# Optimization experiments

Measured on AMD Instinct MI355X. Metric: run time of the kernel, lower is better.

The kernel has to match this reference:

```python
import jax, jax.numpy as jnp
import numpy as np

B, F_C, F_F = 2, 32768, 131072
C_IN, C_OUT, W_DIM, COLOR = 128, 64, 512, 3
K2 = 9
PAD0, PAD1 = 192, 384
ACT_GAIN = float(np.sqrt(2.0))  # lrelu def_gain


def _gather(x, nbr, is_pad, pad):
    # x: [N, C]; nbr: [M, k] indices into [N + pad]; is_pad: [M, k] bool
    padded = jnp.concatenate([x, jnp.zeros((pad, x.shape[1]), x.dtype)], 0)
    g = padded[nbr]  # [M, k, C]
    return jnp.where(is_pad[..., None], jnp.zeros((), x.dtype), g)


def _affine(w, aw, ab):
    # StyleGAN FullyConnectedLayer: runtime weight gain 1/sqrt(fan_in), bias_init=1
    return w @ (aw.T * (1.0 / np.sqrt(aw.shape[1]))) + ab


def _modconv(xg, weight, styles, demodulate=True):
    # xg: [N, k, I]; weight: [O, I, 1, k]; styles: [B, I]
    n, k, ci = xg.shape
    w = weight[:, :, 0, :][None, :, :, :] * styles[:, None, :, None]  # [B,O,I,k]
    if demodulate:
        w = w * jax.lax.rsqrt(jnp.sum(w * w, axis=(2, 3), keepdims=True) + 1e-8)
    xb = xg.reshape(styles.shape[0], -1, k, ci)  # [B,F,k,I]
    return jnp.einsum('bfki,boik->bfo', xb, w).reshape(n, -1)


def _smooth_upsample(x, nbr, is_pad, pad, pool_map):
    # upsample coarse->fine via parent map, then masked neighborhood mean
    xf = x[pool_map]  # [N_fine, C]
    g = _gather(xf, nbr, is_pad, pad)  # [N_fine, k, C]
    cnt = jnp.maximum(jnp.sum(~is_pad, axis=1), 1).astype(x.dtype)
    return jnp.sum(g, axis=1) / cnt[:, None]


def _act(x, gain):
    # clamp_gain(lrelu(x), act_gain*gain, 256*gain)
    y = jnp.where(x >= 0, x, 0.2 * x)
    return jnp.clip(y * (ACT_GAIN * gain), -256.0 * gain, 256.0 * gain)


def setup_inputs():
    key = jax.random.key(0)
    ks = jax.random.split(key, 16)
    x = jax.random.normal(ks[0], (B * F_C, C_IN), jnp.float32)
    img = jax.random.normal(ks[1], (B * F_C, COLOR), jnp.float32)
    ws = jax.random.normal(ks[2], (B, 3, W_DIM), jnp.float32)
    fn0 = jax.random.randint(ks[3], (B * F_C, K2), 0, B * F_C + PAD0, jnp.int32)
    fn1 = jax.random.randint(ks[4], (B * F_F, K2), 0, B * F_F + PAD1, jnp.int32)
    fip0 = jax.random.bernoulli(ks[5], 0.05, (B * F_C, K2))
    fip1 = jax.random.bernoulli(ks[6], 0.05, (B * F_F, K2))
    pool_map0 = jax.random.randint(ks[7], (B * F_F,), 0, B * F_C, jnp.int32)
    a0_w = jax.random.normal(ks[8], (C_IN, W_DIM), jnp.float32)
    a0_b = jnp.ones((C_IN,), jnp.float32)
    W0 = jax.random.normal(ks[9], (C_OUT, C_IN, 1, K2), jnp.float32)
    b0 = jnp.zeros((C_OUT,), jnp.float32)
    ns0 = jnp.zeros((1,), jnp.float32)
    nc0 = jax.random.normal(ks[10], (F_F,), jnp.float32)
    a1_w = jax.random.normal(ks[11], (C_OUT, W_DIM), jnp.float32)
    a1_b = jnp.ones((C_OUT,), jnp.float32)
    W1 = jax.random.normal(ks[12], (C_OUT, C_OUT, 1, K2), jnp.float32)
    b1 = jnp.zeros((C_OUT,), jnp.float32)
    ns1 = jnp.zeros((1,), jnp.float32)
    nc1 = jax.random.normal(ks[13], (F_F,), jnp.float32)
    at_w = jax.random.normal(ks[14], (C_OUT, W_DIM), jnp.float32)
    at_b = jnp.ones((C_OUT,), jnp.float32)
    Wt = jax.random.normal(ks[15], (COLOR, C_OUT, 1, 1), jnp.float32)
    bt = jnp.zeros((COLOR,), jnp.float32)
    return {"x": x, "img": img, "ws": ws, "a0_w": a0_w, "a0_b": a0_b, "W0": W0,
            "b0": b0, "ns0": ns0, "nc0": nc0, "a1_w": a1_w, "a1_b": a1_b,
            "W1": W1, "b1": b1, "ns1": ns1, "nc1": nc1, "at_w": at_w,
            "at_b": at_b, "Wt": Wt, "bt": bt, "fn0": fn0, "fip0": fip0,
            "fn1": fn1, "fip1": fip1, "pool_map0": pool_map0,
            "pad0": PAD0, "pad1": PAD1}


def reference(x, img, ws, a0_w, a0_b, W0, b0, ns0, nc0, a1_w, a1_b, W1, b1, ns1,
              nc1, at_w, at_b, Wt, bt, fn0, fip0, fn1, fip1, pool_map0, pad0, pad1):
    b = ws.shape[0]
    w0, w1, w2 = ws[:, 0], ws[:, 1], ws[:, 2]
    # conv0: coarse gather -> mod conv -> smooth upsample to fine -> noise/bias/act
    s0 = _affine(w0, a0_w, a0_b)
    noise0 = jnp.tile(nc0[None, :], (b, 1)).reshape(-1, 1) * ns0  # noise_mode='const'
    h = _modconv(_gather(x, fn0, fip0, pad0), W0, s0)
    h = _smooth_upsample(h, fn1, fip1, pad1, pool_map0)
    h = _act(h + noise0 + b0[None, :], 1.0)
    # conv1: fine level, no resampler
    s1 = _affine(w1, a1_w, a1_b)
    noise1 = jnp.tile(nc1[None, :], (b, 1)).reshape(-1, 1) * ns1
    h = _modconv(_gather(h, fn1, fip1, pad1), W1, s1)
    h = _act(h + noise1 + b1[None, :], 1.0)
    # torgb: kernel_size=1 -> self index only, no demodulation
    st = _affine(w2, at_w, at_b) * (1.0 / np.sqrt(C_OUT))
    y = _modconv(_gather(h, fn1[:, :1], fip1[:, :1], pad1), Wt, st, demodulate=False)
    y = jnp.clip(y + bt[None, :], -256.0, 256.0)
    img = _smooth_upsample(img, fn1, fip1, pad1, pool_map0) + y
    return (h, img)
```

## Files before the change

kernel.cpp:

```cpp
#include <hip/hip_runtime.h>
#include <hip/hip_bf16.h>

constexpr int F_C   = 32768;
constexpr int F_F   = 131072;
constexpr int N0    = 65536;
constexpr int N1    = 262144;
constexpr int C_IN  = 128;
constexpr int W_DIM = 512;
constexpr int K2c   = 9;
constexpr float RS512     = 0.04419417382415922f;
constexpr float ACT_GAINc = 1.4142135623730951f;

constexpr size_t FO_S0  = 0;
constexpr size_t FO_S1  = 256;
constexpr size_t FO_ST  = 384;
constexpr size_t OFF_WM0T = 2048;
constexpr size_t OFF_WM1T = OFF_WM0T + 294912;
constexpr size_t OFF_H0   = 458752;
constexpr size_t OFF_HA   = OFF_H0 + (size_t)8388608;
constexpr size_t OFF_YPRE = OFF_H0;

typedef short s16x8 __attribute__((ext_vector_type(8)));
typedef float f32x4 __attribute__((ext_vector_type(4)));

__device__ __forceinline__ float b2f(unsigned short u) {
    union { unsigned int i; float f; } v; v.i = ((unsigned int)u) << 16; return v.f;
}
__device__ __forceinline__ unsigned short f2b(float f) {
    __hip_bfloat16 h = __float2bfloat16(f);
    return *reinterpret_cast<unsigned short*>(&h);
}
__device__ __forceinline__ float waveRedSum(float v) {
    for (int m = 32; m; m >>= 1) v += __shfl_xor(v, m, 64);
    return v;
}
__device__ __forceinline__ float actf(float v) {
    float y = (v >= 0.f) ? v : 0.2f * v;
    y *= ACT_GAINc;
    return fminf(fmaxf(y, -256.f), 256.f);
}

__global__ __launch_bounds__(64)
void k_styles(const float* __restrict__ wsF,
              const float* __restrict__ a0w, const float* __restrict__ a0b,
              const float* __restrict__ a1w, const float* __restrict__ a1b,
              const float* __restrict__ atw, const float* __restrict__ atb,
              float* __restrict__ fr)
{
    int bid = blockIdx.x, lane = threadIdx.x;
    int bb, ii, ll, row; const float *aw, *ab; float* dst; float post = 1.f;
    if (bid < 256)      { bb = bid >> 7;             ii = bid & 127; ll = 0; aw = a0w; ab = a0b; dst = fr + FO_S0; row = 128; }
    else if (bid < 384) { int t = bid - 256; bb = t >> 6; ii = t & 63; ll = 1; aw = a1w; ab = a1b; dst = fr + FO_S1; row = 64; }
    else                { int t = bid - 384; bb = t >> 6; ii = t & 63; ll = 2; aw = atw; ab = atb; dst = fr + FO_ST; row = 64; post = 0.125f; }
    const float* wsv = wsF + (size_t)(bb * 3 + ll) * W_DIM;
    const float* awr = aw + (size_t)ii * W_DIM;
    float s = 0.f;
    for (int j = lane; j < W_DIM; j += 64) s += wsv[j] * awr[j];
    s = waveRedSum(s);
    if (lane == 0) dst[bb * row + ii] = (s * RS512 + ab[ii]) * post;
}

__global__ __launch_bounds__(256)
void k_wmod(const float* __restrict__ W0,
            const float* __restrict__ W1,
            const float* __restrict__ fr,
            unsigned short* __restrict__ wm0T,
            unsigned short* __restrict__ wm1T)
{
    int bo = blockIdx.x, tid = threadIdx.x;
    int b, o, CI, NE; const float* W; const float* S; unsigned short* dst;
    if (bo < 128) { b = bo >> 6; o = bo & 63; CI = 128; NE = 1152; W = W0; S = fr + FO_S0; dst = wm0T; }
    else { int t = bo - 128; b = t >> 6; o = t & 63; CI = 64; NE = 576; W = W1; S = fr + FO_S1; dst = wm1T; }
    const float* Wo = W + (size_t)o * NE;
    const float* Sb = S + (size_t)b * CI;
    float ss = 0.f;
    for (int idx = tid; idx < NE; idx += 256) {
        int i = idx / K2c;
        float p = Wo[idx] * Sb[i];
        ss += p * p;
    }
    __shared__ float red[4];
    float s = waveRedSum(ss);
    if ((tid & 63) == 0) red[tid >> 6] = s;
    __syncthreads();
    float d = rsqrtf(red[0] + red[1] + red[2] + red[3] + 1e-8f);
    for (int idx = tid; idx < NE; idx += 256) {
        int i = idx / K2c, kk = idx - i * K2c;
        dst[((size_t)(b * K2c + kk) * 64 + o) * CI + i] = f2b(Wo[idx] * Sb[i] * d);
    }
}

__global__ __launch_bounds__(256)
void k_layer0(const float* __restrict__ xF,
              const int*  __restrict__ fn0,
              const int*  __restrict__ fip0,
              const unsigned short* __restrict__ wm0T,
              unsigned short* __restrict__ h0B)
{
    __shared__ unsigned short A_lds[64 * 136];
    __shared__ unsigned short W_lds[64 * 136];
    __shared__ int snbr[64];
    const int tid  = threadIdx.x;
    const int g0   = blockIdx.x * 64;
    const int b    = g0 / F_C;
    const int wave = tid >> 6, lane = tid & 63;
    const int lg   = lane >> 4, lr = lane & 15;
    f32x4 acc[4] = {};
    for (int kk = 0; kk < K2c; ++kk) {
        __syncthreads();
        if (tid < 64) {
            int g   = g0 + tid;
            int nbr = fn0[(size_t)g * K2c + kk];
            int pd  = fip0[(size_t)g * K2c + kk];
            snbr[tid] = (!pd && nbr < N0) ? nbr : -1;
        }
        __syncthreads();
        {
            int node = tid >> 2, seg = tid & 3;
            int nbr  = snbr[node];
            unsigned short tmp[32];
            if (nbr >= 0) {
                const float4* src = (const float4*)(xF + (size_t)nbr * C_IN + seg * 32);
                #pragma unroll
                for (int q = 0; q < 8; ++q) {
                    float4 f = src[q];
                    tmp[q*4+0] = f2b(f.x); tmp[q*4+1] = f2b(f.y);
                    tmp[q*4+2] = f2b(f.z); tmp[q*4+3] = f2b(f.w);
                }
            } else {
                #pragma unroll
                for (int q = 0; q < 32; ++q) tmp[q] = 0;
            }
            uint4* dstA = (uint4*)(A_lds + node * 136 + seg * 32);
            #pragma unroll
            for (int q = 0; q < 4; ++q) dstA[q] = ((const uint4*)tmp)[q];
            const uint4* wsrc = (const uint4*)(wm0T + ((size_t)(b * K2c + kk) * 64 + node) * C_IN + seg * 32);
            uint4* dstW = (uint4*)(W_lds + node * 136 + seg * 32);
            #pragma unroll
            for (int q = 0; q < 4; ++q) dstW[q] = wsrc[q];
        }
        __syncthreads();
        #pragma unroll
        for (int ks = 0; ks < 4; ++ks) {
            int kb = ks * 32 + lg * 8;
            s16x8 af = *(const s16x8*)(A_lds + (wave * 16 + lr) * 136 + kb);
            #pragma unroll
            for (int nt = 0; nt < 4; ++nt) {
                s16x8 bf = *(const s16x8*)(W_lds + (nt * 16 + lr) * 136 + kb);
                acc[nt] = __builtin_amdgcn_mfma_f32_16x16x32_bf16(af, bf, acc[nt], 0, 0, 0);
            }
        }
    }
    #pragma unroll
    for (int nt = 0; nt < 4; ++nt) {
        int o = nt * 16 + lr;
        #pragma unroll
        for (int r = 0; r < 4; ++r) {
            int node = g0 + wave * 16 + lg * 4 + r;
            h0B[(size_t)node * 64 + o] = f2b(acc[nt][r]);
        }
    }
}

__global__ __launch_bounds__(256)
void k_ha(const unsigned short* __restrict__ h0B,
          const int*  __restrict__ fn1,
          const int*  __restrict__ fip1,
          const int*  __restrict__ pool,
          const float* __restrict__ nc0,
          const float* __restrict__ ns0,
          const float* __restrict__ b0,
          unsigned short* __restrict__ haB)
{
    __shared__ int   pmArr[288];
    __shared__ int   vArr[288];
    __shared__ float invCnt[32];
    const int tid = threadIdx.x;
    const int n0  = blockIdx.x * 32;
    for (int idx = tid; idx < 288; idx += 256) {
        int fn = fn1[(size_t)n0 * K2c + idx];
        int ip = fip1[(size_t)n0 * K2c + idx];
        int v  = !ip;
        int pm = -1;
        if (v && fn < N1) pm = pool[fn];
        pmArr[idx] = pm;
        vArr[idx]  = v;
    }
    __syncthreads();
    if (tid < 32) {
        int c = 0;
        #pragma unroll
        for (int k = 0; k < K2c; ++k) c += vArr[tid * K2c + k];
        invCnt[tid] = 1.f / (float)(c > 0 ? c : 1);
    }
    __syncthreads();
    const int wave = tid >> 6, lane = tid & 63;
    const float nsc  = ns0[0];
    const float bias = b0[lane];
    for (int jj = 0; jj < 8; ++jj) {
        int node = wave * 8 + jj;
        int g    = n0 + node;
        float acc = 0.f;
        #pragma unroll
        for (int k = 0; k < K2c; ++k) {
            int pm = pmArr[node * K2c + k];
            int pc = pm >= 0 ? pm : 0;
            float val = b2f(h0B[(size_t)pc * 64 + lane]);
            acc += (pm >= 0) ? val : 0.f;
        }
        float hu = acc * invCnt[node];
        float v  = hu + nc0[g & (F_F - 1)] * nsc + bias;
        haB[(size_t)g * 64 + lane] = f2b(actf(v));
    }
}

__global__ __launch_bounds__(256)
void k_layer1(const unsigned short* __restrict__ haB,
              const int*  __restrict__ fn1,
              const int*  __restrict__ fip1,
              const unsigned short* __restrict__ wm1T,
              const float* __restrict__ nc1,
              const float* __restrict__ ns1,
              const float* __restrict__ b1,
              const float* __restrict__ stS,
              const float* __restrict__ WtF,
              float* __restrict__ hOut,
              float* __restrict__ yPre2)
{
    __shared__ unsigned short W_lds[2][64 * 72];
    __shared__ int snbr[576];
    const int tid  = threadIdx.x;
    const int g0   = blockIdx.x * 64;
    const int b    = g0 / F_F;
    const int wave = tid >> 6, lane = tid & 63;
    const int lg   = lane >> 4, lr = lane & 15;

    const unsigned short* wtap = wm1T + (size_t)b * K2c * 64 * 64;

    for (int idx = tid; idx < 576; idx += 256) {
        int fn = fn1[(size_t)g0 * K2c + idx];
        int ip = fip1[(size_t)g0 * K2c + idx];
        snbr[idx] = (!ip && fn < N1) ? fn : -1;
    }
    {
        const uint4* src = (const uint4*)wtap;
        int s0 = tid * 2, s1 = s0 + 1;
        uint4 v0 = src[s0], v1 = src[s1];
        *(uint4*)(&W_lds[0][(s0 >> 3) * 72 + (s0 & 7) * 8]) = v0;
        *(uint4*)(&W_lds[0][(s1 >> 3) * 72 + (s1 & 7) * 8]) = v1;
    }
    __syncthreads();

    const int row = wave * 16 + lr;
    int nbrk[9];
    #pragma unroll
    for (int k = 0; k < 9; ++k) nbrk[k] = snbr[row * 9 + k];

    f32x4 acc[4] = {};
    #pragma unroll
    for (int kk = 0; kk < 9; ++kk) {
        const int cur = kk & 1;
        int nbr = nbrk[kk];
        int pc  = nbr >= 0 ? nbr : 0;
        const uint4* ap = (const uint4*)(haB + (size_t)pc * 64) + lg;
        uint4 a0 = ap[0];
        uint4 a1 = ap[4];
        if (nbr < 0) { a0 = uint4{0,0,0,0}; a1 = uint4{0,0,0,0}; }
        if (kk < 8) {
            const uint4* src = (const uint4*)(wtap + (size_t)(kk + 1) * 4096);
            int s0 = tid * 2, s1 = s0 + 1;
            uint4 v0 = src[s0], v1 = src[s1];
            *(uint4*)(&W_lds[cur ^ 1][(s0 >> 3) * 72 + (s0 & 7) * 8]) = v0;
            *(uint4*)(&W_lds[cur ^ 1][(s1 >> 3) * 72 + (s1 & 7) * 8]) = v1;
        }
        s16x8 af0 = *reinterpret_cast<const s16x8*>(&a0);
        s16x8 af1 = *reinterpret_cast<const s16x8*>(&a1);
        #pragma unroll
        for (int nt = 0; nt < 4; ++nt) {
            s16x8 bf0 = *(const s16x8*)(&W_lds[cur][(nt * 16 + lr) * 72 + lg * 8]);
            acc[nt] = __builtin_amdgcn_mfma_f32_16x16x32_bf16(af0, bf0, acc[nt], 0, 0, 0);
        }
        #pragma unroll
        for (int nt = 0; nt < 4; ++nt) {
            s16x8 bf1 = *(const s16x8*)(&W_lds[cur][(nt * 16 + lr) * 72 + 32 + lg * 8]);
            acc[nt] = __builtin_amdgcn_mfma_f32_16x16x32_bf16(af1, bf1, acc[nt], 0, 0, 0);
        }
        __syncthreads();
    }

    float nsc = ns1[0];
    float p00[4] = {}, p01[4] = {}, p02[4] = {};
    float p10[4] = {}, p11[4] = {}, p12[4] = {};
    #pragma unroll
    for (int nt = 0; nt < 4; ++nt) {
        int o = nt * 16 + lr;
        float bias = b1[o];
        float st0  = stS[o], st1 = stS[64 + o];
        float wt0 = WtF[o], wt1 = WtF[64 + o], wt2 = WtF[128 + o];
        float w00 = wt0 * st0, w01 = wt1 * st0, w02 = wt2 * st0;
        float w10 = wt0 * st1, w11 = wt1 * st1, w12 = wt2 * st1;
        #pragma unroll
        for (int r = 0; r < 4; ++r) {
            int node = g0 + wave * 16 + lg * 4 + r;
            float v  = actf(acc[nt][r] + nc1[node & (F_F - 1)] * nsc + bias);
            hOut[(size_t)node * 64 + o] = v;
            p00[r] += v * w00; p01[r] += v * w01; p02[r] += v * w02;
            p10[r] += v * w10; p11[r] += v * w11; p12[r] += v * w12;
        }
    }
    #pragma unroll
    for (int m = 1; m < 16; m <<= 1) {
        #pragma unroll
        for (int r = 0; r < 4; ++r) {
            p00[r] += __shfl_xor(p00[r], m, 64);
            p01[r] += __shfl_xor(p01[r], m, 64);
            p02[r] += __shfl_xor(p02[r], m, 64);
            p10[r] += __shfl_xor(p10[r], m, 64);
            p11[r] += __shfl_xor(p11[r], m, 64);
            p12[r] += __shfl_xor(p12[r], m, 64);
        }
    }
    if (lr == 0) {
        #pragma unroll
        for (int r = 0; r < 4; ++r) {
            int node = g0 + wave * 16 + lg * 4 + r;
            yPre2[(size_t)node * 6 + 0] = p00[r];
            yPre2[(size_t)node * 6 + 1] = p01[r];
            yPre2[(size_t)node * 6 + 2] = p02[r];
            yPre2[(size_t)node * 6 + 3] = p10[r];
            yPre2[(size_t)node * 6 + 4] = p11[r];
            yPre2[(size_t)node * 6 + 5] = p12[r];
        }
    }
}

__global__ __launch_bounds__(256)
void k_rgb(const float* __restrict__ yPre2,
           const float* __restrict__ imgF,
           const int*  __restrict__ fn1,
           const int*  __restrict__ fip1,
           const int*  __restrict__ pool,
           const float* __restrict__ btF,
           float* __restrict__ outImg)
{
    const int n = blockIdx.x * 256 + threadIdx.x;
    const int bOut = n / F_F;
    int fn[K2c], ip[K2c];
    #pragma unroll
    for (int k = 0; k < K2c; ++k) {
        fn[k] = fn1[(size_t)n * K2c + k];
        ip[k] = fip1[(size_t)n * K2c + k];
    }
    int pm[K2c], cnt = 0;
    #pragma unroll
    for (int k = 0; k < K2c; ++k) {
        int v  = !ip[k];
        cnt   += v;
        pm[k]  = (v && fn[k] < N1) ? pool[fn[k]] : -1;
    }
    float sr = 0.f, sg = 0.f, sb = 0.f;
    #pragma unroll
    for (int k = 0; k < K2c; ++k) {
        int   pc = pm[k] >= 0 ? pm[k] : 0;
        float m  = pm[k] >= 0 ? 1.f : 0.f;
        sr += m * imgF[(size_t)pc * 3 + 0];
        sg += m * imgF[(size_t)pc * 3 + 1];
        sb += m * imgF[(size_t)pc * 3 + 2];
    }
    int nb0 = (!ip[0] && fn[0] < N1) ? fn[0] : -1;
    float y0 = 0.f, y1 = 0.f, y2 = 0.f;
    if (nb0 >= 0) {
        const float* yp = yPre2 + (size_t)nb0 * 6 + bOut * 3;
        y0 = yp[0]; y1 = yp[1]; y2 = yp[2];
    }
    float ic = 1.f / (float)(cnt > 0 ? cnt : 1);
    y0 = fminf(fmaxf(y0 + btF[0], -256.f), 256.f);
    y1 = fminf(fmaxf(y1 + btF[1], -256.f), 256.f);
    y2 = fminf(fmaxf(y2 + btF[2], -256.f), 256.f);
    outImg[(size_t)n * 3 + 0] = sr * ic + y0;
    outImg[(size_t)n * 3 + 1] = sg * ic + y1;
    outImg[(size_t)n * 3 + 2] = sb * ic + y2;
}

extern "C" void kernel_launch(void* const* d_in, const int* in_sizes, int n_in,
                              void* d_out, int out_size, void* d_ws, size_t ws_size,
                              hipStream_t stream)
{
    const float* xF   = (const float*)d_in[0];
    const float* imgF = (const float*)d_in[1];
    const float* wsF  = (const float*)d_in[2];
    const float* a0w  = (const float*)d_in[3];
    const float* a0b  = (const float*)d_in[4];
    const float* W0w  = (const float*)d_in[5];
    const float* b0w  = (const float*)d_in[6];
    const float* ns0  = (const float*)d_in[7];
    const float* nc0  = (const float*)d_in[8];
    const float* a1w  = (const float*)d_in[9];
    const float* a1b  = (const float*)d_in[10];
    const float* W1w  = (const float*)d_in[11];
    const float* b1w  = (const float*)d_in[12];
    const float* ns1  = (const float*)d_in[13];
    const float* nc1  = (const float*)d_in[14];
    const float* atw  = (const float*)d_in[15];
    const float* atb  = (const float*)d_in[16];
    const float* WtF  = (const float*)d_in[17];
    const float* btF  = (const float*)d_in[18];
    const int* fn0  = (const int*)d_in[19];
    const int* fip0 = (const int*)d_in[20];
    const int* fn1  = (const int*)d_in[21];
    const int* fip1 = (const int*)d_in[22];
    const int* pool = (const int*)d_in[23];

    char* wsb = (char*)d_ws;
    float* fr = (float*)wsb;
    unsigned short* wm0T = (unsigned short*)(wsb + OFF_WM0T);
    unsigned short* wm1T = (unsigned short*)(wsb + OFF_WM1T);
    unsigned short* h0B  = (unsigned short*)(wsb + OFF_H0);
    unsigned short* haB  = (unsigned short*)(wsb + OFF_HA);
    float* yPre2         = (float*)(wsb + OFF_YPRE);

    float* hOut   = (float*)d_out;
    float* imgOut = hOut + (size_t)N1 * 64;

    hipLaunchKernelGGL(k_styles, dim3(512), dim3(64), 0, stream,
                       wsF, a0w, a0b, a1w, a1b, atw, atb, fr);
    hipLaunchKernelGGL(k_wmod, dim3(256), dim3(256), 0, stream,
                       W0w, W1w, fr, wm0T, wm1T);
    hipLaunchKernelGGL(k_layer0, dim3(N0 / 64), dim3(256), 0, stream,
                       xF, fn0, fip0, wm0T, h0B);
    hipLaunchKernelGGL(k_ha, dim3(N1 / 32), dim3(256), 0, stream,
                       h0B, fn1, fip1, pool, nc0, ns0, b0w, haB);
    hipLaunchKernelGGL(k_layer1, dim3(N1 / 64), dim3(256), 0, stream,
                       haB, fn1, fip1, wm1T, nc1, ns1, b1w,
                       fr + FO_ST, WtF, hOut, yPre2);
    hipLaunchKernelGGL(k_rgb, dim3(N1 / 256), dim3(256), 0, stream,
                       yPre2, imgF, fn1, fip1, pool, btF, imgOut);
}
```

Before: 201.3 us.

## Gather bf16 activations directly into registers and read weights from global

Adds a pre-pass that converts the fp32 input x to bf16 once. Layer0 then gathers neighbor rows straight into MFMA A-fragments in registers instead of staging them through LDS, and it reads the modulated weights straight from global/L2. Layer1 likewise drops its LDS double-buffered weight staging and all per-tap barriers, loading weight fragments from global. Both kernels get a min-blocks-per-CU occupancy hint. The aim is to remove LDS traffic and synchronisation, at the cost of redundant per-wave weight loads from cache and an extra conversion kernel.

```diff
diff --git a/kernel.cpp b/kernel.cpp
--- a/kernel.cpp
+++ b/kernel.cpp
@@ -19,6 +19,7 @@
 constexpr size_t OFF_H0   = 458752;
 constexpr size_t OFF_HA   = OFF_H0 + (size_t)8388608;
 constexpr size_t OFF_YPRE = OFF_H0;
+constexpr size_t OFF_XB   = OFF_HA;
 
 typedef short s16x8 __attribute__((ext_vector_type(8)));
 typedef float f32x4 __attribute__((ext_vector_type(4)));
@@ -91,62 +92,55 @@
 }
 
 __global__ __launch_bounds__(256)
-void k_layer0(const float* __restrict__ xF,
+void k_xcvt(const float* __restrict__ xF, unsigned short* __restrict__ xB)
+{
+    int i = blockIdx.x * 256 + threadIdx.x;
+    float4 f = ((const float4*)xF)[i];
+    union { unsigned short u[4]; uint2 v; } t;
+    t.u[0] = f2b(f.x); t.u[1] = f2b(f.y); t.u[2] = f2b(f.z); t.u[3] = f2b(f.w);
+    ((uint2*)xB)[i] = t.v;
+}
+
+__global__ __launch_bounds__(256, 4)
+void k_layer0(const unsigned short* __restrict__ xB,
               const int*  __restrict__ fn0,
               const int*  __restrict__ fip0,
               const unsigned short* __restrict__ wm0T,
               unsigned short* __restrict__ h0B)
 {
-    __shared__ unsigned short A_lds[64 * 136];
-    __shared__ unsigned short W_lds[64 * 136];
-    __shared__ int snbr[64];
     const int tid  = threadIdx.x;
     const int g0   = blockIdx.x * 64;
     const int b    = g0 / F_C;
     const int wave = tid >> 6, lane = tid & 63;
     const int lg   = lane >> 4, lr = lane & 15;
+    const int row  = g0 + wave * 16 + lr;
+    const unsigned short* wtap = wm0T + (size_t)b * K2c * 64 * C_IN;
+
+    int nbrk[9];
+    #pragma unroll
+    for (int k = 0; k < 9; ++k) {
+        int fn = fn0[(size_t)row * 9 + k];
+        int ip = fip0[(size_t)row * 9 + k];
+        nbrk[k] = (!ip && fn < N0) ? fn : -1;
+    }
+
     f32x4 acc[4] = {};
-    for (int kk = 0; kk < K2c; ++kk) {
-        __syncthreads();
-        if (tid < 64) {
-            int g   = g0 + tid;
-            int nbr = fn0[(size_t)g * K2c + kk];
-            int pd  = fip0[(size_t)g * K2c + kk];
-            snbr[tid] = (!pd && nbr < N0) ? nbr : -1;
-        }
-        __syncthreads();
-        {
-            int node = tid >> 2, seg = tid & 3;
-            int nbr  = snbr[node];
-            unsigned short tmp[32];
-            if (nbr >= 0) {
-                const float4* src = (const float4*)(xF + (size_t)nbr * C_IN + seg * 32);
-                #pragma unroll
-                for (int q = 0; q < 8; ++q) {
-                    float4 f = src[q];
-                    tmp[q*4+0] = f2b(f.x); tmp[q*4+1] = f2b(f.y);
-                    tmp[q*4+2] = f2b(f.z); tmp[q*4+3] = f2b(f.w);
-                }
-            } else {
-                #pragma unroll
-                for (int q = 0; q < 32; ++q) tmp[q] = 0;
-            }
-            uint4* dstA = (uint4*)(A_lds + node * 136 + seg * 32);
-            #pragma unroll
-            for (int q = 0; q < 4; ++q) dstA[q] = ((const uint4*)tmp)[q];
-            const uint4* wsrc = (const uint4*)(wm0T + ((size_t)(b * K2c + kk) * 64 + node) * C_IN + seg * 32);
-            uint4* dstW = (uint4*)(W_lds + node * 136 + seg * 32);
-            #pragma unroll
-            for (int q = 0; q < 4; ++q) dstW[q] = wsrc[q];
-        }
-        __syncthreads();
+    #pragma unroll
+    for (int kk = 0; kk < 9; ++kk) {
+        int nbr = nbrk[kk];
+        int pc  = nbr >= 0 ? nbr : 0;
+        const uint4* ap = (const uint4*)(xB + (size_t)pc * C_IN) + lg;
+        uint4 a[4];
+        #pragma unroll
+        for (int ks = 0; ks < 4; ++ks) a[ks] = ap[ks * 4];
+        if (nbr < 0) { a[0] = a[1] = a[2] = a[3] = uint4{0,0,0,0}; }
+        const unsigned short* wk = wtap + (size_t)kk * 64 * C_IN;
         #pragma unroll
         for (int ks = 0; ks < 4; ++ks) {
-            int kb = ks * 32 + lg * 8;
-            s16x8 af = *(const s16x8*)(A_lds + (wave * 16 + lr) * 136 + kb);
+            s16x8 af = *reinterpret_cast<const s16x8*>(&a[ks]);
             #pragma unroll
             for (int nt = 0; nt < 4; ++nt) {
-                s16x8 bf = *(const s16x8*)(W_lds + (nt * 16 + lr) * 136 + kb);
+                s16x8 bf = *(const s16x8*)(wk + (nt * 16 + lr) * C_IN + ks * 32 + lg * 8);
                 acc[nt] = __builtin_amdgcn_mfma_f32_16x16x32_bf16(af, bf, acc[nt], 0, 0, 0);
             }
         }
@@ -214,7 +208,7 @@
     }
 }
 
-__global__ __launch_bounds__(256)
+__global__ __launch_bounds__(256, 4)
 void k_layer1(const unsigned short* __restrict__ haB,
               const int*  __restrict__ fn1,
               const int*  __restrict__ fip1,
@@ -227,65 +221,44 @@
               float* __restrict__ hOut,
               float* __restrict__ yPre2)
 {
-    __shared__ unsigned short W_lds[2][64 * 72];
-    __shared__ int snbr[576];
     const int tid  = threadIdx.x;
     const int g0   = blockIdx.x * 64;
     const int b    = g0 / F_F;
     const int wave = tid >> 6, lane = tid & 63;
     const int lg   = lane >> 4, lr = lane & 15;
-
+    const int row  = g0 + wave * 16 + lr;
     const unsigned short* wtap = wm1T + (size_t)b * K2c * 64 * 64;
 
-    for (int idx = tid; idx < 576; idx += 256) {
-        int fn = fn1[(size_t)g0 * K2c + idx];
-        int ip = fip1[(size_t)g0 * K2c + idx];
-        snbr[idx] = (!ip && fn < N1) ? fn : -1;
-    }
-    {
-        const uint4* src = (const uint4*)wtap;
-        int s0 = tid * 2, s1 = s0 + 1;
-        uint4 v0 = src[s0], v1 = src[s1];
-        *(uint4*)(&W_lds[0][(s0 >> 3) * 72 + (s0 & 7) * 8]) = v0;
-        *(uint4*)(&W_lds[0][(s1 >> 3) * 72 + (s1 & 7) * 8]) = v1;
-    }
-    __syncthreads();
-
-    const int row = wave * 16 + lr;
     int nbrk[9];
     #pragma unroll
-    for (int k = 0; k < 9; ++k) nbrk[k] = snbr[row * 9 + k];
+    for (int k = 0; k < 9; ++k) {
+        int fn = fn1[(size_t)row * 9 + k];
+        int ip = fip1[(size_t)row * 9 + k];
+        nbrk[k] = (!ip && fn < N1) ? fn : -1;
+    }
 
     f32x4 acc[4] = {};
     #pragma unroll
     for (int kk = 0; kk < 9; ++kk) {
-        const int cur = kk & 1;
         int nbr = nbrk[kk];
         int pc  = nbr >= 0 ? nbr : 0;
         const uint4* ap = (const uint4*)(haB + (size_t)pc * 64) + lg;
         uint4 a0 = ap[0];
         uint4 a1 = ap[4];
         if (nbr < 0) { a0 = uint4{0,0,0,0}; a1 = uint4{0,0,0,0}; }
-        if (kk < 8) {
-            const uint4* src = (const uint4*)(wtap + (size_t)(kk + 1) * 4096);
-            int s0 = tid * 2, s1 = s0 + 1;
-            uint4 v0 = src[s0], v1 = src[s1];
-            *(uint4*)(&W_lds[cur ^ 1][(s0 >> 3) * 72 + (s0 & 7) * 8]) = v0;
-            *(uint4*)(&W_lds[cur ^ 1][(s1 >> 3) * 72 + (s1 & 7) * 8]) = v1;
-        }
+        const unsigned short* wk = wtap + (size_t)kk * 4096;
         s16x8 af0 = *reinterpret_cast<const s16x8*>(&a0);
         s16x8 af1 = *reinterpret_cast<const s16x8*>(&a1);
         #pragma unroll
         for (int nt = 0; nt < 4; ++nt) {
-            s16x8 bf0 = *(const s16x8*)(&W_lds[cur][(nt * 16 + lr) * 72 + lg * 8]);
+            s16x8 bf0 = *(const s16x8*)(wk + (nt * 16 + lr) * 64 + lg * 8);
             acc[nt] = __builtin_amdgcn_mfma_f32_16x16x32_bf16(af0, bf0, acc[nt], 0, 0, 0);
         }
         #pragma unroll
         for (int nt = 0; nt < 4; ++nt) {
-            s16x8 bf1 = *(const s16x8*)(&W_lds[cur][(nt * 16 + lr) * 72 + 32 + lg * 8]);
+            s16x8 bf1 = *(const s16x8*)(wk + (nt * 16 + lr) * 64 + 32 + lg * 8);
             acc[nt] = __builtin_amdgcn_mfma_f32_16x16x32_bf16(af1, bf1, acc[nt], 0, 0, 0);
         }
-        __syncthreads();
     }
 
     float nsc = ns1[0];
@@ -417,6 +390,7 @@
     unsigned short* wm1T = (unsigned short*)(wsb + OFF_WM1T);
     unsigned short* h0B  = (unsigned short*)(wsb + OFF_H0);
     unsigned short* haB  = (unsigned short*)(wsb + OFF_HA);
+    unsigned short* xB   = (unsigned short*)(wsb + OFF_XB);
     float* yPre2         = (float*)(wsb + OFF_YPRE);
 
     float* hOut   = (float*)d_out;
@@ -426,8 +400,10 @@
                        wsF, a0w, a0b, a1w, a1b, atw, atb, fr);
     hipLaunchKernelGGL(k_wmod, dim3(256), dim3(256), 0, stream,
                        W0w, W1w, fr, wm0T, wm1T);
+    hipLaunchKernelGGL(k_xcvt, dim3((N0 * C_IN) / 4 / 256), dim3(256), 0, stream,
+                       xF, xB);
     hipLaunchKernelGGL(k_layer0, dim3(N0 / 64), dim3(256), 0, stream,
-                       xF, fn0, fip0, wm0T, h0B);
+                       xB, fn0, fip0, wm0T, h0B);
     hipLaunchKernelGGL(k_ha, dim3(N1 / 32), dim3(256), 0, stream,
                        h0B, fn1, fip1, pool, nc0, ns0, b0w, haB);
     hipLaunchKernelGGL(k_layer1, dim3(N1 / 64), dim3(256), 0, stream,
```

Result: slower. 340.2 us (+69.1%).

## Preload all conv1 tap weights into swizzled LDS and process 256 nodes per block

Applied to the files above, without the earlier changes.

k_layer1 now loads all nine 64x64 tap weight tiles into LDS once, using an XOR swizzle in place of padding, instead of double-buffering one tap at a time with a barrier per tap. Each block handles 256 nodes (64 per wave), so each B fragment read from LDS is reused across four row groups. The per-tap __syncthreads are gone, and neighbor indices are read straight from global memory into registers. In exchange the kernel needs 72KB of LDS and far more accumulator and neighbor registers, which lowers occupancy and leaves less latency hiding for the gathered loads.

```diff
diff --git a/kernel.cpp b/kernel.cpp
--- a/kernel.cpp
+++ b/kernel.cpp
@@ -214,7 +214,7 @@
     }
 }
 
-__global__ __launch_bounds__(256)
+__global__ __launch_bounds__(256, 2)
 void k_layer1(const unsigned short* __restrict__ haB,
               const int*  __restrict__ fn1,
               const int*  __restrict__ fip1,
@@ -227,109 +227,112 @@
               float* __restrict__ hOut,
               float* __restrict__ yPre2)
 {
-    __shared__ unsigned short W_lds[2][64 * 72];
-    __shared__ int snbr[576];
+    __shared__ unsigned short W_lds[9 * 64 * 64];
     const int tid  = threadIdx.x;
-    const int g0   = blockIdx.x * 64;
+    const int g0   = blockIdx.x * 256;
     const int b    = g0 / F_F;
     const int wave = tid >> 6, lane = tid & 63;
     const int lg   = lane >> 4, lr = lane & 15;
-
-    const unsigned short* wtap = wm1T + (size_t)b * K2c * 64 * 64;
-
-    for (int idx = tid; idx < 576; idx += 256) {
-        int fn = fn1[(size_t)g0 * K2c + idx];
-        int ip = fip1[(size_t)g0 * K2c + idx];
-        snbr[idx] = (!ip && fn < N1) ? fn : -1;
-    }
-    {
-        const uint4* src = (const uint4*)wtap;
-        int s0 = tid * 2, s1 = s0 + 1;
-        uint4 v0 = src[s0], v1 = src[s1];
-        *(uint4*)(&W_lds[0][(s0 >> 3) * 72 + (s0 & 7) * 8]) = v0;
-        *(uint4*)(&W_lds[0][(s1 >> 3) * 72 + (s1 & 7) * 8]) = v1;
+    const int wbase = g0 + wave * 64;
+    const unsigned short* wtap = wm1T + (size_t)b * K2c * 4096;
+
+    #pragma unroll
+    for (int t = 0; t < 18; ++t) {
+        int idx = tid + 256 * t;
+        int tap = idx >> 9;
+        int rem = idx & 511;
+        int row = rem >> 3, c = rem & 7;
+        uint4 v = ((const uint4*)wtap)[idx];
+        *(uint4*)(&W_lds[tap * 4096 + row * 64 + ((c ^ (row & 7)) << 3)]) = v;
+    }
+
+    int nbrk[4][9];
+    #pragma unroll
+    for (int rg = 0; rg < 4; ++rg) {
+        int row = wbase + rg * 16 + lr;
+        #pragma unroll
+        for (int k = 0; k < 9; ++k) {
+            int fn = fn1[(size_t)row * 9 + k];
+            int ip = fip1[(size_t)row * 9 + k];
+            nbrk[rg][k] = (!ip && fn < N1) ? fn : -1;
+        }
     }
     __syncthreads();
 
-    const int row = wave * 16 + lr;
-    int nbrk[9];
-    #pragma unroll
-    for (int k = 0; k < 9; ++k) nbrk[k] = snbr[row * 9 + k];
-
-    f32x4 acc[4] = {};
+    f32x4 acc[4][4] = {};
     #pragma unroll
     for (int kk = 0; kk < 9; ++kk) {
-        const int cur = kk & 1;
-        int nbr = nbrk[kk];
-        int pc  = nbr >= 0 ? nbr : 0;
-        const uint4* ap = (const uint4*)(haB + (size_t)pc * 64) + lg;
-        uint4 a0 = ap[0];
-        uint4 a1 = ap[4];
-        if (nbr < 0) { a0 = uint4{0,0,0,0}; a1 = uint4{0,0,0,0}; }
-        if (kk < 8) {
-            const uint4* src = (const uint4*)(wtap + (size_t)(kk + 1) * 4096);
-            int s0 = tid * 2, s1 = s0 + 1;
-            uint4 v0 = src[s0], v1 = src[s1];
-            *(uint4*)(&W_lds[cur ^ 1][(s0 >> 3) * 72 + (s0 & 7) * 8]) = v0;
-            *(uint4*)(&W_lds[cur ^ 1][(s1 >> 3) * 72 + (s1 & 7) * 8]) = v1;
-        }
-        s16x8 af0 = *reinterpret_cast<const s16x8*>(&a0);
-        s16x8 af1 = *reinterpret_cast<const s16x8*>(&a1);
+        s16x8 bf[2][4];
+        #pragma unroll
+        for (int h = 0; h < 2; ++h)
+            #pragma unroll
+            for (int nt = 0; nt < 4; ++nt) {
+                int row = nt * 16 + lr;
+                bf[h][nt] = *(const s16x8*)(&W_lds[kk * 4096 + row * 64 + (((h * 4 + lg) ^ (row & 7)) << 3)]);
+            }
+        #pragma unroll
+        for (int rg = 0; rg < 4; ++rg) {
+            int nbr = nbrk[rg][kk];
+            int pc  = nbr >= 0 ? nbr : 0;
+            const uint4* ap = (const uint4*)(haB + (size_t)pc * 64) + lg;
+            uint4 a0 = ap[0], a1 = ap[4];
+            if (nbr < 0) { a0 = uint4{0,0,0,0}; a1 = uint4{0,0,0,0}; }
+            s16x8 af0 = *reinterpret_cast<const s16x8*>(&a0);
+            s16x8 af1 = *reinterpret_cast<const s16x8*>(&a1);
+            #pragma unroll
+            for (int nt = 0; nt < 4; ++nt)
+                acc[rg][nt] = __builtin_amdgcn_mfma_f32_16x16x32_bf16(af0, bf[0][nt], acc[rg][nt], 0, 0, 0);
+            #pragma unroll
+            for (int nt = 0; nt < 4; ++nt)
+                acc[rg][nt] = __builtin_amdgcn_mfma_f32_16x16x32_bf16(af1, bf[1][nt], acc[rg][nt], 0, 0, 0);
+        }
+    }
+
+    const float nsc = ns1[0];
+    #pragma unroll
+    for (int rg = 0; rg < 4; ++rg) {
+        float p00[4] = {}, p01[4] = {}, p02[4] = {};
+        float p10[4] = {}, p11[4] = {}, p12[4] = {};
         #pragma unroll
         for (int nt = 0; nt < 4; ++nt) {
-            s16x8 bf0 = *(const s16x8*)(&W_lds[cur][(nt * 16 + lr) * 72 + lg * 8]);
-            acc[nt] = __builtin_amdgcn_mfma_f32_16x16x32_bf16(af0, bf0, acc[nt], 0, 0, 0);
-        }
-        #pragma unroll
-        for (int nt = 0; nt < 4; ++nt) {
-            s16x8 bf1 = *(const s16x8*)(&W_lds[cur][(nt * 16 + lr) * 72 + 32 + lg * 8]);
-            acc[nt] = __builtin_amdgcn_mfma_f32_16x16x32_bf16(af1, bf1, acc[nt], 0, 0, 0);
-        }
-        __syncthreads();
-    }
-
-    float nsc = ns1[0];
-    float p00[4] = {}, p01[4] = {}, p02[4] = {};
-    float p10[4] = {}, p11[4] = {}, p12[4] = {};
-    #pragma unroll
-    for (int nt = 0; nt < 4; ++nt) {
-        int o = nt * 16 + lr;
-        float bias = b1[o];
-        float st0  = stS[o], st1 = stS[64 + o];
-        float wt0 = WtF[o], wt1 = WtF[64 + o], wt2 = WtF[128 + o];
-        float w00 = wt0 * st0, w01 = wt1 * st0, w02 = wt2 * st0;
-        float w10 = wt0 * st1, w11 = wt1 * st1, w12 = wt2 * st1;
-        #pragma unroll
-        for (int r = 0; r < 4; ++r) {
-            int node = g0 + wave * 16 + lg * 4 + r;
-            float v  = actf(acc[nt][r] + nc1[node & (F_F - 1)] * nsc + bias);
-            hOut[(size_t)node * 64 + o] = v;
-            p00[r] += v * w00; p01[r] += v * w01; p02[r] += v * w02;
-            p10[r] += v * w10; p11[r] += v * w11; p12[r] += v * w12;
-        }
-    }
-    #pragma unroll
-    for (int m = 1; m < 16; m <<= 1) {
-        #pragma unroll
-        for (int r = 0; r < 4; ++r) {
-            p00[r] += __shfl_xor(p00[r], m, 64);
-            p01[r] += __shfl_xor(p01[r], m, 64);
-            p02[r] += __shfl_xor(p02[r], m, 64);
-            p10[r] += __shfl_xor(p10[r], m, 64);
-            p11[r] += __shfl_xor(p11[r], m, 64);
-            p12[r] += __shfl_xor(p12[r], m, 64);
-        }
-    }
-    if (lr == 0) {
-        #pragma unroll
-        for (int r = 0; r < 4; ++r) {
-            int node = g0 + wave * 16 + lg * 4 + r;
-            yPre2[(size_t)node * 6 + 0] = p00[r];
-            yPre2[(size_t)node * 6 + 1] = p01[r];
-            yPre2[(size_t)node * 6 + 2] = p02[r];
-            yPre2[(size_t)node * 6 + 3] = p10[r];
-            yPre2[(size_t)node * 6 + 4] = p11[r];
-            yPre2[(size_t)node * 6 + 5] = p12[r];
+            int o = nt * 16 + lr;
+            float bias = b1[o];
+            float st0  = stS[o], st1 = stS[64 + o];
+            float wt0 = WtF[o], wt1 = WtF[64 + o], wt2 = WtF[128 + o];
+            float w00 = wt0 * st0, w01 = wt1 * st0, w02 = wt2 * st0;
+            float w10 = wt0 * st1, w11 = wt1 * st1, w12 = wt2 * st1;
+            #pragma unroll
+            for (int r = 0; r < 4; ++r) {
+                int node = wbase + rg * 16 + lg * 4 + r;
+                float v  = actf(acc[rg][nt][r] + nc1[node & (F_F - 1)] * nsc + bias);
+                hOut[(size_t)node * 64 + o] = v;
+                p00[r] += v * w00; p01[r] += v * w01; p02[r] += v * w02;
+                p10[r] += v * w10; p11[r] += v * w11; p12[r] += v * w12;
+            }
+        }
+        #pragma unroll
+        for (int m = 1; m < 16; m <<= 1) {
+            #pragma unroll
+            for (int r = 0; r < 4; ++r) {
+                p00[r] += __shfl_xor(p00[r], m, 64);
+                p01[r] += __shfl_xor(p01[r], m, 64);
+                p02[r] += __shfl_xor(p02[r], m, 64);
+                p10[r] += __shfl_xor(p10[r], m, 64);
+                p11[r] += __shfl_xor(p11[r], m, 64);
+                p12[r] += __shfl_xor(p12[r], m, 64);
+            }
+        }
+        if (lr == 0) {
+            #pragma unroll
+            for (int r = 0; r < 4; ++r) {
+                int node = wbase + rg * 16 + lg * 4 + r;
+                yPre2[(size_t)node * 6 + 0] = p00[r];
+                yPre2[(size_t)node * 6 + 1] = p01[r];
+                yPre2[(size_t)node * 6 + 2] = p02[r];
+                yPre2[(size_t)node * 6 + 3] = p10[r];
+                yPre2[(size_t)node * 6 + 4] = p11[r];
+                yPre2[(size_t)node * 6 + 5] = p12[r];
+            }
         }
     }
 }
@@ -430,7 +433,7 @@
                        xF, fn0, fip0, wm0T, h0B);
     hipLaunchKernelGGL(k_ha, dim3(N1 / 32), dim3(256), 0, stream,
                        h0B, fn1, fip1, pool, nc0, ns0, b0w, haB);
-    hipLaunchKernelGGL(k_layer1, dim3(N1 / 64), dim3(256), 0, stream,
+    hipLaunchKernelGGL(k_layer1, dim3(N1 / 256), dim3(256), 0, stream,
                        haB, fn1, fip1, wm1T, nc1, ns1, b1w,
                        fr + FO_ST, WtF, hOut, yPre2);
     hipLaunchKernelGGL(k_rgb, dim3(N1 / 256), dim3(256), 0, stream,
```

Measured after the change: 200.0 us. About the same (-0.6%).
